# Kernel tuning notes

Measured on AMD Instinct MI355X. Metric: run time of the kernel, lower is better.

## Reference

```python
import jax, jax.numpy as jnp
import numpy as np


def setup_inputs() -> dict:
    key = jax.random.key(0)
    ks = jax.random.split(key, 8)
    B, C, H, W = 4, 256, 56, 56
    Cq = C // 8
    s = 0.05  # small init scale for conv weights, like kaiming-ish for 1x1 convs
    return {
        "x": jax.random.normal(ks[0], (B, C, H, W), jnp.float32),
        "Wq": jax.random.normal(ks[1], (Cq, C), jnp.float32) * s,
        "bq": jax.random.normal(ks[2], (Cq,), jnp.float32) * s,
        "Wk": jax.random.normal(ks[3], (Cq, C), jnp.float32) * s,
        "bk": jax.random.normal(ks[4], (Cq,), jnp.float32) * s,
        "Wv": jax.random.normal(ks[5], (C, C), jnp.float32) * s,
        "bv": jax.random.normal(ks[6], (C,), jnp.float32) * s,
        "gamma": jax.random.normal(ks[7], (1,), jnp.float32),
    }


def reference(x, Wq, bq, Wk, bk, Wv, bv, gamma):
    B, C, H, W = x.shape
    N = H * W
    xf = x.reshape(B, C, N)  # flatten spatial

    # 1x1 convs == channel matmuls
    q = jnp.einsum('oc,bcn->bon', Wq, xf) + bq[None, :, None]   # [B,Cq,N]
    k = jnp.einsum('oc,bcn->bon', Wk, xf) + bk[None, :, None]   # [B,Cq,N]
    v = jnp.einsum('oc,bcn->bon', Wv, xf) + bv[None, :, None]   # [B,C,N]

    # lipschitz_norm from weights: u=||Q||_F, v=max row-norm of K^T, w=max row-norm of V^T
    u = jnp.linalg.norm(Wq)
    vn = jnp.max(jnp.linalg.norm(Wk.T, axis=1))
    wn = jnp.max(jnp.linalg.norm(Wv.T, axis=1))
    norm_value = jnp.maximum(u * vn, u * wn)  # maximum(u*v, v*u, u*w)

    # energy[b,i,j] = <q[:,i], k[:,j]>, scaled by custom Lipschitz norm
    energy = jnp.einsum('bci,bcj->bij', q, k) / norm_value      # [B,N,N]
    attention = jax.nn.softmax(energy, axis=-1)

    # out[b,c,i] = sum_j v[b,c,j] * attention[b,i,j]
    out = jnp.einsum('bcj,bij->bci', v, attention).reshape(B, C, H, W)

    # lipschitz_bound: exp(sqrt(3)) * sqrt(N/C) + 2*sqrt(6)
    bound = np.float32(np.exp(np.sqrt(3.0)) * np.sqrt(N / C) + 2.0 * np.sqrt(6.0))
    out = out / bound

    return gamma * out + x
```

## Files before the change

### kernel.cpp

```cpp
#include <hip/hip_runtime.h>

#define N_SP 3136
#define C_CH 256
#define CQ   32
#define NB   4
#define JT   64
#define NJT  49
#define QT   64
#define INV_BOUND 0.04051569f
#define LOG2E 1.44269504f

typedef __attribute__((ext_vector_type(8))) short bf16x8;
typedef __attribute__((ext_vector_type(4))) float f32x4;
typedef __attribute__((ext_vector_type(2))) long long l64x2;
typedef unsigned short u16;
typedef unsigned int   u32;
typedef unsigned char  u8;
typedef long long      l64;

#define MFMA16(a,b,c) __builtin_amdgcn_mfma_f32_16x16x32_bf16(a,b,c,0,0,0)
#define MFMA8(a,b,c)  __builtin_amdgcn_mfma_f32_16x16x32_bf8_fp8(a,b,c,0,0,0)

__device__ __forceinline__ u16 f2b(float f) {
    u32 u = __builtin_bit_cast(u32, f);
    u += 0x7fffu + ((u >> 16) & 1u);
    return (u16)(u >> 16);
}
__device__ __forceinline__ u8 f2fp8(float f) {
    return (u8)(__builtin_amdgcn_cvt_pk_fp8_f32(f, f, 0, false) & 0xff);
}
__device__ __forceinline__ void dma16(const void* g, void* l) {
    __builtin_amdgcn_global_load_lds((const __attribute__((address_space(1))) u32*)g,
                                     (__attribute__((address_space(3))) u32*)l, 16, 0, 0);
}

__global__ __launch_bounds__(256) void stage0_kernel(
    const float* __restrict__ Wq, const float* __restrict__ Wk,
    const float* __restrict__ Wv, u8* __restrict__ Wqb,
    u8* __restrict__ Wkb, u8* __restrict__ Wvb,
    float* __restrict__ scale_out, float* __restrict__ kmax)
{
    __shared__ float red[256];
    const int t = threadIdx.x;
    const int bid = blockIdx.x;

    if (bid < 80) {
        int idx = bid * 256 + t;
        const float* src; u8* dst; int off;
        if (idx < 2048)      { src = Wq; dst = Wqb; off = idx; }
        else if (idx < 4096) { src = Wk; dst = Wkb; off = idx - 2048; }
        else                 { src = Wv; dst = Wvb; off = idx - 4096; }
        float4 v = *(const float4*)(src + off * 4);
        ushort4 o; o.x = f2b(v.x); o.y = f2b(v.y); o.z = f2b(v.z); o.w = f2b(v.w);
        const int row = off >> 6, inner = (off & 63) * 8;
        *(ushort4*)(dst + row * 512 + (inner ^ ((row & 15) << 5))) = o;
    } else {
        if (t < NB) kmax[t] = 0.f;
        float u2 = 0.f;
        for (int i = t; i < CQ * C_CH; i += 256) { float w = Wq[i]; u2 += w * w; }
        red[t] = u2; __syncthreads();
        #pragma unroll
        for (int s = 128; s > 0; s >>= 1) { if (t < s) red[t] += red[t + s]; __syncthreads(); }
        float u2t = red[0]; __syncthreads();
        float vn2 = 0.f;
        for (int o = 0; o < CQ; ++o)   { float w = Wk[o * C_CH + t]; vn2 += w * w; }
        float wn2 = 0.f;
        for (int o = 0; o < C_CH; ++o) { float w = Wv[o * C_CH + t]; wn2 += w * w; }
        red[t] = fmaxf(vn2, wn2); __syncthreads();
        #pragma unroll
        for (int s = 128; s > 0; s >>= 1) { if (t < s) red[t] = fmaxf(red[t], red[t + s]); __syncthreads(); }
        if (t == 0) scale_out[0] = 1.0f / (sqrtf(u2t) * sqrtf(red[0]));
    }
}

__global__ __launch_bounds__(512) void qkv_fused(
    const float* __restrict__ x, const u8* __restrict__ Wqb,
    const u8* __restrict__ Wkb, const u8* __restrict__ Wvb,
    const float* __restrict__ bq, const float* __restrict__ bk,
    const float* __restrict__ bv, const float* __restrict__ scale_p,
    u16* __restrict__ qT, u8* __restrict__ Kg, u8* __restrict__ Vg,
    float* __restrict__ qnorm, float* __restrict__ kmax)
{
    __shared__ __align__(16) u8 smem[147712];
    u8* const xTl = smem;
    float* const ftile = (float*)(smem + 32768);
    u8* const W0 = smem + 49408;
    u8* const W1 = smem + 82176;

    const int t = threadIdx.x;
    const int w = t >> 6, lane = t & 63, li = t & 15, g = (t >> 4) & 3;
    const int wq = w & 3, wh = w >> 2;
    const int b  = blockIdx.x / NJT;
    const int nt = blockIdx.x % NJT;
    const int n0 = nt * 64;
    const f32x4 zero = {0.f, 0.f, 0.f, 0.f};

    #pragma unroll
    for (int k = 0; k < 2; ++k)
        dma16(Wqb + k * 8192 + t * 16, W0 + k * 8192 + w * 1024);
    #pragma unroll
    for (int k = 0; k < 2; ++k)
        dma16(Wkb + k * 8192 + t * 16, W0 + 16384 + k * 8192 + w * 1024);
    #pragma unroll
    for (int k = 0; k < 8; ++k)
        dma16(Wvb + k * 8192 + t * 16, W1 + k * 8192 + w * 1024);

    #pragma unroll 1
    for (int sl = 0; sl < 4; ++sl) {
        const int c0 = sl * 64;
        if (t < 256) {
            const int cc = t >> 4, nn4 = (t & 15) * 4;
            #pragma unroll
            for (int k = 0; k < 4; ++k) {
                int cl = cc + k * 16;
                float4 v = *(const float4*)(x + (size_t)(b * C_CH + c0 + cl) * N_SP + n0 + nn4);
                ftile[cl * 65 + nn4]     = v.x;
                ftile[cl * 65 + nn4 + 1] = v.y;
                ftile[cl * 65 + nn4 + 2] = v.z;
                ftile[cl * 65 + nn4 + 3] = v.w;
            }
        }
        __syncthreads();
        if (t < 256) {
            const int c4 = (t & 15) * 4, nn = t >> 4;
            #pragma unroll
            for (int k = 0; k < 4; ++k) {
                int nl = nn + k * 16;
                ushort4 o;
                o.x = f2b(ftile[(c4 + 0) * 65 + nl]);
                o.y = f2b(ftile[(c4 + 1) * 65 + nl]);
                o.z = f2b(ftile[(c4 + 2) * 65 + nl]);
                o.w = f2b(ftile[(c4 + 3) * 65 + nl]);
                *(ushort4*)(xTl + nl * 512 + (((c0 + c4) * 2) ^ ((nl & 15) << 5))) = o;
            }
        }
        __syncthreads();
    }

    asm volatile("s_waitcnt vmcnt(0) lgkmcnt(0)" ::: "memory");
    __syncthreads();

    const int swz = li << 5;
    const int n = n0 + wq * 16 + li;
    bf16x8 xf[8];
    #pragma unroll
    for (int ks = 0; ks < 8; ++ks)
        xf[ks] = *(const bf16x8*)(xTl + (wq * 16 + li) * 512 + ((ks * 64 + 16 * g) ^ swz));

    if (wh == 0) {
        f32x4 aq0 = zero, aq1 = zero;
        #pragma unroll
        for (int ks = 0; ks < 8; ++ks) {
            const int o = (ks * 64 + 16 * g) ^ swz;
            bf16x8 w0 = *(const bf16x8*)(W0 + li * 512 + o);
            bf16x8 w1 = *(const bf16x8*)(W0 + (16 + li) * 512 + o);
            aq0 = MFMA16(w0, xf[ks], aq0);
            aq1 = MFMA16(w1, xf[ks], aq1);
        }
        const float scf = scale_p[0] * LOG2E;
        f32x4 bq0 = *(const f32x4*)(bq + 4 * g);
        f32x4 bq1 = *(const f32x4*)(bq + 16 + 4 * g);
        float qn2 = 0.f;
        ushort4 s0, s1;
        #pragma unroll
        for (int r = 0; r < 4; ++r) {
            float q0 = (aq0[r] + bq0[r]) * scf;
            float q1 = (aq1[r] + bq1[r]) * scf;
            qn2 += q0 * q0 + q1 * q1;
            ((u16*)&s0)[r] = f2b(q0); ((u16*)&s1)[r] = f2b(q1);
        }
        *(ushort4*)(qT + (size_t)(b * N_SP + n) * CQ + 4 * g)      = s0;
        *(ushort4*)(qT + (size_t)(b * N_SP + n) * CQ + 16 + 4 * g) = s1;
        qn2 += __shfl_xor(qn2, 16); qn2 += __shfl_xor(qn2, 32);
        if (g == 0) qnorm[b * N_SP + n] = sqrtf(qn2);
    } else {
        f32x4 ak0 = zero, ak1 = zero;
        #pragma unroll
        for (int ks = 0; ks < 8; ++ks) {
            const int o = (ks * 64 + 16 * g) ^ swz;
            bf16x8 w2 = *(const bf16x8*)(W0 + 16384 + li * 512 + o);
            bf16x8 w3 = *(const bf16x8*)(W0 + 16384 + (16 + li) * 512 + o);
            ak0 = MFMA16(w2, xf[ks], ak0);
            ak1 = MFMA16(w3, xf[ks], ak1);
        }
        f32x4 bk0 = *(const f32x4*)(bk + 4 * g);
        f32x4 bk1 = *(const f32x4*)(bk + 16 + 4 * g);
        float kn2 = 0.f;
        ushort4 s0, s1;
        #pragma unroll
        for (int r = 0; r < 4; ++r) {
            float k0 = ak0[r] + bk0[r];
            float k1 = ak1[r] + bk1[r];
            kn2 += k0 * k0 + k1 * k1;
            ((u16*)&s0)[r] = f2b(k0); ((u16*)&s1)[r] = f2b(k1);
        }
        u8* krow = Kg + ((size_t)b * N_SP + n) * 64;
        const int swn = ((n >> 1) & 3) << 4;
        *(ushort4*)(krow + ((8 * g) ^ swn))      = s0;
        *(ushort4*)(krow + ((32 + 8 * g) ^ swn)) = s1;
        kn2 += __shfl_xor(kn2, 16); kn2 += __shfl_xor(kn2, 32);
        float kn = sqrtf(kn2);
        #pragma unroll
        for (int d = 1; d < 16; d <<= 1) kn = fmaxf(kn, __shfl_xor(kn, d));
        if (lane == 0) atomicMax((int*)(kmax + b), __float_as_int(kn));
    }

    const int jj = wq * 16 + li;
    const int p = ((jj >> 5) & 1) * 8 + ((jj >> 3) & 3) * 16 + (jj & 7);
    u8* vtile = Vg + (size_t)(b * NJT + nt) * 16384;
    {
        const int r0 = wh * 64;
        f32x4 a[4] = {zero, zero, zero, zero};
        #pragma unroll
        for (int ks = 0; ks < 8; ++ks) {
            const int o = (ks * 64 + 16 * g) ^ swz;
            #pragma unroll
            for (int fr = 0; fr < 4; ++fr) {
                bf16x8 wf = *(const bf16x8*)(W1 + (size_t)(r0 + fr * 16 + li) * 512 + o);
                a[fr] = MFMA16(wf, xf[ks], a[fr]);
            }
        }
        #pragma unroll
        for (int fr = 0; fr < 4; ++fr) {
            f32x4 bb = *(const f32x4*)(bv + r0 + fr * 16 + 4 * g);
            #pragma unroll
            for (int r = 0; r < 4; ++r) {
                const int c = r0 + fr * 16 + 4 * g + r;
                vtile[c * 64 + (p ^ (((c >> 1) & 3) << 4))] = f2fp8(a[fr][r] + bb[r]);
            }
        }
    }

    __syncthreads();
    #pragma unroll
    for (int k = 0; k < 8; ++k)
        dma16(Wvb + 65536 + k * 8192 + t * 16, W1 + k * 8192 + w * 1024);
    asm volatile("s_waitcnt vmcnt(0)" ::: "memory");
    __syncthreads();

    {
        const int r0v = 128 + wh * 64;
        const int r0l = wh * 64;
        f32x4 a[4] = {zero, zero, zero, zero};
        #pragma unroll
        for (int ks = 0; ks < 8; ++ks) {
            const int o = (ks * 64 + 16 * g) ^ swz;
            #pragma unroll
            for (int fr = 0; fr < 4; ++fr) {
                bf16x8 wf = *(const bf16x8*)(W1 + (size_t)(r0l + fr * 16 + li) * 512 + o);
                a[fr] = MFMA16(wf, xf[ks], a[fr]);
            }
        }
        #pragma unroll
        for (int fr = 0; fr < 4; ++fr) {
            f32x4 bb = *(const f32x4*)(bv + r0v + fr * 16 + 4 * g);
            #pragma unroll
            for (int r = 0; r < 4; ++r) {
                const int c = r0v + fr * 16 + 4 * g + r;
                vtile[c * 64 + (p ^ (((c >> 1) & 3) << 4))] = f2fp8(a[fr][r] + bb[r]);
            }
        }
    }
}

__global__ __launch_bounds__(1024) void attn_mfma(
    const u16* __restrict__ qT, const u8* __restrict__ Kg,
    const u8* __restrict__ Vg, const float* __restrict__ x,
    const float* __restrict__ gamma_p, const float* __restrict__ qnorm,
    const float* __restrict__ kmax, float* __restrict__ out)
{
    __shared__ __align__(16) u8 smem[90112];
    u8* const Vl = smem;
    u8* const Kl = smem + 65536;
    u8* const Pl = smem + 81920;

    const int t = threadIdx.x;
    const int w = t >> 6, li = t & 15, g = (t >> 4) & 3;
    const int jh = w & 3, qh = w >> 2;
    const int swz = ((li >> 1) & 3) << 4;

    const int b  = blockIdx.x / NJT;
    const int qt = blockIdx.x % NJT;
    const int i0 = qt * QT;

    const u16* qTb = qT + (size_t)b * N_SP * CQ;
    const u8*  Kbb = Kg + (size_t)b * N_SP * 64;
    const u8*  Vbb = Vg + (size_t)b * NJT * 16384;
    const float kmb = kmax[b];
    const f32x4 zero = {0.f, 0.f, 0.f, 0.f};

    const bf16x8 qf = *(const bf16x8*)(qTb + (size_t)(i0 + qh * 16 + li) * CQ + 8 * g);
    const float  mr = qnorm[b * N_SP + i0 + qh * 16 + li] * kmb;

    f32x4 acc[4];
    #pragma unroll
    for (int qq = 0; qq < 4; ++qq) acc[qq] = zero;
    float ls = 0.f;

    #define ISSUE(jt_, s_) do {                                               \
        dma16(Vbb + (size_t)(jt_) * 16384 + t * 16,                           \
              Vl + (s_) * 16384 + w * 1024);                                  \
        if (t < 256)                                                          \
            dma16(Kbb + (size_t)(jt_) * 4096 + t * 16,                        \
                  Kl + (s_) * 4096 + w * 1024);                               \
    } while (0)

    #define SPHASE(it_) do {                                                  \
        const u8* Kc_ = Kl + ((it_) & 3) * 4096;                              \
        bf16x8 kf_ = *(const bf16x8*)(Kc_ + (jh * 16 + li) * 64 + ((16 * g) ^ swz)); \
        f32x4 s_ = MFMA16(kf_, qf, zero);                                     \
        float a0_ = exp2f(s_[0] - mr), a1_ = exp2f(s_[1] - mr);               \
        float a2_ = exp2f(s_[2] - mr), a3_ = exp2f(s_[3] - mr);               \
        ls += (a0_ + a1_) + (a2_ + a3_);                                      \
        int pk_ = __builtin_amdgcn_cvt_pk_bf8_f32(a0_, a1_, 0, false);        \
        pk_ = __builtin_amdgcn_cvt_pk_bf8_f32(a2_, a3_, pk_, true);           \
        *(u32*)(Pl + ((it_) & 1) * 4096 + (qh * 16 + li) * 64 + (p0 ^ swz)) = (u32)pk_; \
    } while (0)

    #define PVPHASE(it_) do {                                                 \
        const u8* Pp_ = Pl + ((it_) & 1) * 4096;                              \
        const u8* Vc_ = Vl + ((it_) & 3) * 16384;                             \
        __builtin_amdgcn_s_setprio(1);                                        \
        l64x2 pa0_ = *(const l64x2*)(Pp_ + (0 * 16 + li) * 64 + ((16 * g) ^ swz)); \
        l64x2 pa1_ = *(const l64x2*)(Pp_ + (1 * 16 + li) * 64 + ((16 * g) ^ swz)); \
        l64x2 pa2_ = *(const l64x2*)(Pp_ + (2 * 16 + li) * 64 + ((16 * g) ^ swz)); \
        l64x2 pa3_ = *(const l64x2*)(Pp_ + (3 * 16 + li) * 64 + ((16 * g) ^ swz)); \
        l64x2 v0_  = *(const l64x2*)(Vc_ + (w * 16 + li) * 64 + ((16 * g) ^ swz)); \
        acc[0] = MFMA8(pa0_[0], v0_[0], acc[0]);                              \
        acc[1] = MFMA8(pa1_[0], v0_[0], acc[1]);                              \
        acc[2] = MFMA8(pa2_[0], v0_[0], acc[2]);                              \
        acc[3] = MFMA8(pa3_[0], v0_[0], acc[3]);                              \
        acc[0] = MFMA8(pa0_[1], v0_[1], acc[0]);                              \
        acc[1] = MFMA8(pa1_[1], v0_[1], acc[1]);                              \
        acc[2] = MFMA8(pa2_[1], v0_[1], acc[2]);                              \
        acc[3] = MFMA8(pa3_[1], v0_[1], acc[3]);                              \
        __builtin_amdgcn_s_setprio(0);                                        \
    } while (0)

    ISSUE(0, 0);
    ISSUE(1, 1);

    const int p0 = ((jh >> 1) & 1) * 8 + ((jh * 2 + (g >> 1)) & 3) * 16 + 4 * (g & 1);

    if (w < 4) asm volatile("s_waitcnt vmcnt(2) lgkmcnt(0)" ::: "memory");
    else       asm volatile("s_waitcnt vmcnt(1) lgkmcnt(0)" ::: "memory");
    __builtin_amdgcn_s_barrier();
    asm volatile("" ::: "memory");
    ISSUE(2, 2);
    SPHASE(0);

    for (int it = 1; it < NJT; ++it) {
        if (w < 4) asm volatile("s_waitcnt vmcnt(2) lgkmcnt(0)" ::: "memory");
        else       asm volatile("s_waitcnt vmcnt(1) lgkmcnt(0)" ::: "memory");
        __builtin_amdgcn_s_barrier();
        asm volatile("" ::: "memory");
        {
            int jn = it + 2; if (jn > NJT - 1) jn = NJT - 1;
            ISSUE(jn, (it + 2) & 3);
        }
        PVPHASE(it - 1);
        SPHASE(it);
    }

    asm volatile("s_waitcnt lgkmcnt(0)" ::: "memory");
    __builtin_amdgcn_s_barrier();
    asm volatile("" ::: "memory");
    PVPHASE(NJT - 1);
    #undef ISSUE
    #undef SPHASE
    #undef PVPHASE

    ls += __shfl_xor(ls, 16); ls += __shfl_xor(ls, 32);
    __syncthreads();
    float* red       = (float*)Pl;
    float* red_final = (float*)(Pl + 1024);
    if ((t & 63) < 16) red[w * 16 + li] = ls;
    __syncthreads();
    if (t < 64) {
        const int qh2 = t >> 4, l2 = t & 15;
        float s = red[(qh2 * 4 + 0) * 16 + l2] + red[(qh2 * 4 + 1) * 16 + l2]
                + red[(qh2 * 4 + 2) * 16 + l2] + red[(qh2 * 4 + 3) * 16 + l2];
        red_final[t] = s;
    }
    __syncthreads();

    const float gsc = gamma_p[0] * INV_BOUND;
    const int c = w * 16 + li;
    #pragma unroll
    for (int qq = 0; qq < 4; ++qq) {
        f32x4 lsv = *(const f32x4*)(red_final + qq * 16 + 4 * g);
        f32x4 rinv;
        #pragma unroll
        for (int r = 0; r < 4; ++r) rinv[r] = gsc / lsv[r];
        const size_t base = ((size_t)b * C_CH + c) * N_SP + i0 + qq * 16 + 4 * g;
        float4 xv = *(const float4*)(x + base);
        float4 o;
        o.x = acc[qq][0] * rinv[0] + xv.x;
        o.y = acc[qq][1] * rinv[1] + xv.y;
        o.z = acc[qq][2] * rinv[2] + xv.z;
        o.w = acc[qq][3] * rinv[3] + xv.w;
        *(float4*)(out + base) = o;
    }
}

extern "C" void kernel_launch(void* const* d_in, const int* in_sizes, int n_in,
                              void* d_out, int out_size, void* d_ws, size_t ws_size,
                              hipStream_t stream)
{
    const float* x  = (const float*)d_in[0];
    const float* Wq = (const float*)d_in[1];
    const float* bq = (const float*)d_in[2];
    const float* Wk = (const float*)d_in[3];
    const float* bk = (const float*)d_in[4];
    const float* Wv = (const float*)d_in[5];
    const float* bv = (const float*)d_in[6];
    const float* gm = (const float*)d_in[7];
    float* out = (float*)d_out;
    float* ws  = (float*)d_ws;

    float* scale = ws;
    float* kmax  = ws + 4;
    float* qnorm = ws + 8;
    u8* Wqb = (u8*)(ws + 8 + NB * N_SP);
    u8* Wkb = Wqb + 32 * 512;
    u8* Wvb = Wkb + 32 * 512;
    u16* qT = (u16*)(Wvb + 256 * 512);
    u8* Kg  = (u8*)(qT + (size_t)NB * N_SP * CQ);
    u8* Vg  = Kg + (size_t)NB * N_SP * 64;

    stage0_kernel<<<81, 256, 0, stream>>>(Wq, Wk, Wv, Wqb, Wkb, Wvb, scale, kmax);
    qkv_fused<<<NB * NJT, 512, 0, stream>>>(x, Wqb, Wkb, Wvb, bq, bk, bv, scale, qT, Kg, Vg, qnorm, kmax);
    attn_mfma<<<NB * NJT, 1024, 0, stream>>>(qT, Kg, Vg, x, gm, qnorm, kmax, out);
}
```

Baseline: 81.32 us.

## Widen qkv_fused to 1024 threads with parallel x transpose and overlapped Wv load

The QKV projection kernel now runs 16 waves instead of 8. All four 64-channel slices of x are transposed into LDS at once rather than in a sequential four-pass loop. The first half of Wv is loaded by DMA into the freed staging buffer while Q/K are computed, and V rows are split across twice as many waves. This aims to cut the serial transpose latency and hide the weight load, at the cost of higher register pressure per thread under a 1024-thread launch bound and reuse of the staging buffer.

Measured after the change: 79.74 us (median of 2 runs). No clear change (-1.9%).

```diff
diff --git a/kernel.cpp b/kernel.cpp
--- a/kernel.cpp
+++ b/kernel.cpp
@@ -73,7 +73,7 @@
     }
 }
 
-__global__ __launch_bounds__(512) void qkv_fused(
+__global__ __launch_bounds__(1024) void qkv_fused(
     const float* __restrict__ x, const u8* __restrict__ Wqb,
     const u8* __restrict__ Wkb, const u8* __restrict__ Wvb,
     const float* __restrict__ bq, const float* __restrict__ bk,
@@ -81,15 +81,14 @@
     u16* __restrict__ qT, u8* __restrict__ Kg, u8* __restrict__ Vg,
     float* __restrict__ qnorm, float* __restrict__ kmax)
 {
-    __shared__ __align__(16) u8 smem[147712];
+    __shared__ __align__(16) u8 smem[132096];
     u8* const xTl = smem;
-    float* const ftile = (float*)(smem + 32768);
-    u8* const W0 = smem + 49408;
-    u8* const W1 = smem + 82176;
+    u8* const FW  = smem + 32768;
+    u8* const W0  = smem + 99328;
 
     const int t = threadIdx.x;
     const int w = t >> 6, lane = t & 63, li = t & 15, g = (t >> 4) & 3;
-    const int wq = w & 3, wh = w >> 2;
+    const int wq = w & 3;
     const int b  = blockIdx.x / NJT;
     const int nt = blockIdx.x % NJT;
     const int n0 = nt * 64;
@@ -97,48 +96,40 @@
 
     #pragma unroll
     for (int k = 0; k < 2; ++k)
-        dma16(Wqb + k * 8192 + t * 16, W0 + k * 8192 + w * 1024);
-    #pragma unroll
-    for (int k = 0; k < 2; ++k)
-        dma16(Wkb + k * 8192 + t * 16, W0 + 16384 + k * 8192 + w * 1024);
-    #pragma unroll
-    for (int k = 0; k < 8; ++k)
-        dma16(Wvb + k * 8192 + t * 16, W1 + k * 8192 + w * 1024);
-
-    #pragma unroll 1
-    for (int sl = 0; sl < 4; ++sl) {
+        dma16((k == 0 ? Wqb : Wkb) + t * 16, W0 + k * 16384 + w * 1024);
+
+    {
+        const int sl = t >> 8, tt = t & 255;
         const int c0 = sl * 64;
-        if (t < 256) {
-            const int cc = t >> 4, nn4 = (t & 15) * 4;
-            #pragma unroll
-            for (int k = 0; k < 4; ++k) {
-                int cl = cc + k * 16;
-                float4 v = *(const float4*)(x + (size_t)(b * C_CH + c0 + cl) * N_SP + n0 + nn4);
-                ftile[cl * 65 + nn4]     = v.x;
-                ftile[cl * 65 + nn4 + 1] = v.y;
-                ftile[cl * 65 + nn4 + 2] = v.z;
-                ftile[cl * 65 + nn4 + 3] = v.w;
-            }
+        float* ftile = (float*)(FW + sl * 16640);
+        const int cc = tt >> 4, nn4 = (tt & 15) * 4;
+        #pragma unroll
+        for (int k = 0; k < 4; ++k) {
+            int cl = cc + k * 16;
+            float4 v = *(const float4*)(x + (size_t)(b * C_CH + c0 + cl) * N_SP + n0 + nn4);
+            ftile[cl * 65 + nn4]     = v.x;
+            ftile[cl * 65 + nn4 + 1] = v.y;
+            ftile[cl * 65 + nn4 + 2] = v.z;
+            ftile[cl * 65 + nn4 + 3] = v.w;
         }
         __syncthreads();
-        if (t < 256) {
-            const int c4 = (t & 15) * 4, nn = t >> 4;
-            #pragma unroll
-            for (int k = 0; k < 4; ++k) {
-                int nl = nn + k * 16;
-                ushort4 o;
-                o.x = f2b(ftile[(c4 + 0) * 65 + nl]);
-                o.y = f2b(ftile[(c4 + 1) * 65 + nl]);
-                o.z = f2b(ftile[(c4 + 2) * 65 + nl]);
-                o.w = f2b(ftile[(c4 + 3) * 65 + nl]);
-                *(ushort4*)(xTl + nl * 512 + (((c0 + c4) * 2) ^ ((nl & 15) << 5))) = o;
-            }
-        }
-        __syncthreads();
-    }
-
-    asm volatile("s_waitcnt vmcnt(0) lgkmcnt(0)" ::: "memory");
-    __syncthreads();
+        const int c4 = (tt & 15) * 4, nn = tt >> 4;
+        #pragma unroll
+        for (int k = 0; k < 4; ++k) {
+            int nl = nn + k * 16;
+            ushort4 o;
+            o.x = f2b(ftile[(c4 + 0) * 65 + nl]);
+            o.y = f2b(ftile[(c4 + 1) * 65 + nl]);
+            o.z = f2b(ftile[(c4 + 2) * 65 + nl]);
+            o.w = f2b(ftile[(c4 + 3) * 65 + nl]);
+            *(ushort4*)(xTl + nl * 512 + (((c0 + c4) * 2) ^ ((nl & 15) << 5))) = o;
+        }
+    }
+    __syncthreads();
+
+    #pragma unroll
+    for (int k = 0; k < 4; ++k)
+        dma16(Wvb + k * 16384 + t * 16, FW + k * 16384 + w * 1024);
 
     const int swz = li << 5;
     const int n = n0 + wq * 16 + li;
@@ -147,81 +138,93 @@
     for (int ks = 0; ks < 8; ++ks)
         xf[ks] = *(const bf16x8*)(xTl + (wq * 16 + li) * 512 + ((ks * 64 + 16 * g) ^ swz));
 
-    if (wh == 0) {
-        f32x4 aq0 = zero, aq1 = zero;
-        #pragma unroll
-        for (int ks = 0; ks < 8; ++ks) {
-            const int o = (ks * 64 + 16 * g) ^ swz;
-            bf16x8 w0 = *(const bf16x8*)(W0 + li * 512 + o);
-            bf16x8 w1 = *(const bf16x8*)(W0 + (16 + li) * 512 + o);
-            aq0 = MFMA16(w0, xf[ks], aq0);
-            aq1 = MFMA16(w1, xf[ks], aq1);
-        }
-        const float scf = scale_p[0] * LOG2E;
-        f32x4 bq0 = *(const f32x4*)(bq + 4 * g);
-        f32x4 bq1 = *(const f32x4*)(bq + 16 + 4 * g);
-        float qn2 = 0.f;
-        ushort4 s0, s1;
-        #pragma unroll
-        for (int r = 0; r < 4; ++r) {
-            float q0 = (aq0[r] + bq0[r]) * scf;
-            float q1 = (aq1[r] + bq1[r]) * scf;
-            qn2 += q0 * q0 + q1 * q1;
-            ((u16*)&s0)[r] = f2b(q0); ((u16*)&s1)[r] = f2b(q1);
-        }
-        *(ushort4*)(qT + (size_t)(b * N_SP + n) * CQ + 4 * g)      = s0;
-        *(ushort4*)(qT + (size_t)(b * N_SP + n) * CQ + 16 + 4 * g) = s1;
-        qn2 += __shfl_xor(qn2, 16); qn2 += __shfl_xor(qn2, 32);
-        if (g == 0) qnorm[b * N_SP + n] = sqrtf(qn2);
-    } else {
-        f32x4 ak0 = zero, ak1 = zero;
-        #pragma unroll
-        for (int ks = 0; ks < 8; ++ks) {
-            const int o = (ks * 64 + 16 * g) ^ swz;
-            bf16x8 w2 = *(const bf16x8*)(W0 + 16384 + li * 512 + o);
-            bf16x8 w3 = *(const bf16x8*)(W0 + 16384 + (16 + li) * 512 + o);
-            ak0 = MFMA16(w2, xf[ks], ak0);
-            ak1 = MFMA16(w3, xf[ks], ak1);
-        }
-        f32x4 bk0 = *(const f32x4*)(bk + 4 * g);
-        f32x4 bk1 = *(const f32x4*)(bk + 16 + 4 * g);
-        float kn2 = 0.f;
-        ushort4 s0, s1;
-        #pragma unroll
-        for (int r = 0; r < 4; ++r) {
-            float k0 = ak0[r] + bk0[r];
-            float k1 = ak1[r] + bk1[r];
-            kn2 += k0 * k0 + k1 * k1;
-            ((u16*)&s0)[r] = f2b(k0); ((u16*)&s1)[r] = f2b(k1);
-        }
-        u8* krow = Kg + ((size_t)b * N_SP + n) * 64;
-        const int swn = ((n >> 1) & 3) << 4;
-        *(ushort4*)(krow + ((8 * g) ^ swn))      = s0;
-        *(ushort4*)(krow + ((32 + 8 * g) ^ swn)) = s1;
-        kn2 += __shfl_xor(kn2, 16); kn2 += __shfl_xor(kn2, 32);
-        float kn = sqrtf(kn2);
-        #pragma unroll
-        for (int d = 1; d < 16; d <<= 1) kn = fmaxf(kn, __shfl_xor(kn, d));
-        if (lane == 0) atomicMax((int*)(kmax + b), __float_as_int(kn));
-    }
+    asm volatile("s_waitcnt vmcnt(4) lgkmcnt(0)" ::: "memory");
+    __builtin_amdgcn_s_barrier();
+    asm volatile("" ::: "memory");
+
+    const int wh = w >> 2;
+    if (w < 8) {
+        if (wh == 0) {
+            f32x4 aq0 = zero, aq1 = zero;
+            #pragma unroll
+            for (int ks = 0; ks < 8; ++ks) {
+                const int o = (ks * 64 + 16 * g) ^ swz;
+                bf16x8 w0 = *(const bf16x8*)(W0 + li * 512 + o);
+                bf16x8 w1 = *(const bf16x8*)(W0 + (16 + li) * 512 + o);
+                aq0 = MFMA16(w0, xf[ks], aq0);
+                aq1 = MFMA16(w1, xf[ks], aq1);
+            }
+            const float scf = scale_p[0] * LOG2E;
+            f32x4 bq0 = *(const f32x4*)(bq + 4 * g);
+            f32x4 bq1 = *(const f32x4*)(bq + 16 + 4 * g);
+            float qn2 = 0.f;
+            ushort4 s0, s1;
+            #pragma unroll
+            for (int r = 0; r < 4; ++r) {
+                float q0 = (aq0[r] + bq0[r]) * scf;
+                float q1 = (aq1[r] + bq1[r]) * scf;
+                qn2 += q0 * q0 + q1 * q1;
+                ((u16*)&s0)[r] = f2b(q0); ((u16*)&s1)[r] = f2b(q1);
+            }
+            *(ushort4*)(qT + (size_t)(b * N_SP + n) * CQ + 4 * g)      = s0;
+            *(ushort4*)(qT + (size_t)(b * N_SP + n) * CQ + 16 + 4 * g) = s1;
+            qn2 += __shfl_xor(qn2, 16); qn2 += __shfl_xor(qn2, 32);
+            if (g == 0) qnorm[b * N_SP + n] = sqrtf(qn2);
+        } else {
+            f32x4 ak0 = zero, ak1 = zero;
+            #pragma unroll
+            for (int ks = 0; ks < 8; ++ks) {
+                const int o = (ks * 64 + 16 * g) ^ swz;
+                bf16x8 w2 = *(const bf16x8*)(W0 + 16384 + li * 512 + o);
+                bf16x8 w3 = *(const bf16x8*)(W0 + 16384 + (16 + li) * 512 + o);
+                ak0 = MFMA16(w2, xf[ks], ak0);
+                ak1 = MFMA16(w3, xf[ks], ak1);
+            }
+            f32x4 bk0 = *(const f32x4*)(bk + 4 * g);
+            f32x4 bk1 = *(const f32x4*)(bk + 16 + 4 * g);
+            float kn2 = 0.f;
+            ushort4 s0, s1;
+            #pragma unroll
+            for (int r = 0; r < 4; ++r) {
+                float k0 = ak0[r] + bk0[r];
+                float k1 = ak1[r] + bk1[r];
+                kn2 += k0 * k0 + k1 * k1;
+                ((u16*)&s0)[r] = f2b(k0); ((u16*)&s1)[r] = f2b(k1);
+            }
+            u8* krow = Kg + ((size_t)b * N_SP + n) * 64;
+            const int swn = ((n >> 1) & 3) << 4;
+            *(ushort4*)(krow + ((8 * g) ^ swn))      = s0;
+            *(ushort4*)(krow + ((32 + 8 * g) ^ swn)) = s1;
+            kn2 += __shfl_xor(kn2, 16); kn2 += __shfl_xor(kn2, 32);
+            float kn = sqrtf(kn2);
+            #pragma unroll
+            for (int d = 1; d < 16; d <<= 1) kn = fmaxf(kn, __shfl_xor(kn, d));
+            if (lane == 0) atomicMax((int*)(kmax + b), __float_as_int(kn));
+        }
+    }
+
+    asm volatile("s_waitcnt vmcnt(0)" ::: "memory");
+    __builtin_amdgcn_s_barrier();
+    asm volatile("" ::: "memory");
 
     const int jj = wq * 16 + li;
     const int p = ((jj >> 5) & 1) * 8 + ((jj >> 3) & 3) * 16 + (jj & 7);
     u8* vtile = Vg + (size_t)(b * NJT + nt) * 16384;
+    const int vg = w >> 2;
     {
-        const int r0 = wh * 64;
-        f32x4 a[4] = {zero, zero, zero, zero};
+        const int r0 = vg * 32;
+        f32x4 a[2] = {zero, zero};
         #pragma unroll
         for (int ks = 0; ks < 8; ++ks) {
             const int o = (ks * 64 + 16 * g) ^ swz;
             #pragma unroll
-            for (int fr = 0; fr < 4; ++fr) {
-                bf16x8 wf = *(const bf16x8*)(W1 + (size_t)(r0 + fr * 16 + li) * 512 + o);
+            for (int fr = 0; fr < 2; ++fr) {
+                bf16x8 wf = *(const bf16x8*)(FW + (size_t)(r0 + fr * 16 + li) * 512 + o);
                 a[fr] = MFMA16(wf, xf[ks], a[fr]);
             }
         }
         #pragma unroll
-        for (int fr = 0; fr < 4; ++fr) {
+        for (int fr = 0; fr < 2; ++fr) {
             f32x4 bb = *(const f32x4*)(bv + r0 + fr * 16 + 4 * g);
             #pragma unroll
             for (int r = 0; r < 4; ++r) {
@@ -233,26 +236,25 @@
 
     __syncthreads();
     #pragma unroll
-    for (int k = 0; k < 8; ++k)
-        dma16(Wvb + 65536 + k * 8192 + t * 16, W1 + k * 8192 + w * 1024);
+    for (int k = 0; k < 4; ++k)
+        dma16(Wvb + 65536 + k * 16384 + t * 16, FW + k * 16384 + w * 1024);
     asm volatile("s_waitcnt vmcnt(0)" ::: "memory");
     __syncthreads();
-
     {
-        const int r0v = 128 + wh * 64;
-        const int r0l = wh * 64;
-        f32x4 a[4] = {zero, zero, zero, zero};
+        const int r0v = 128 + vg * 32;
+        const int r0l = vg * 32;
+        f32x4 a[2] = {zero, zero};
         #pragma unroll
         for (int ks = 0; ks < 8; ++ks) {
             const int o = (ks * 64 + 16 * g) ^ swz;
             #pragma unroll
-            for (int fr = 0; fr < 4; ++fr) {
-                bf16x8 wf = *(const bf16x8*)(W1 + (size_t)(r0l + fr * 16 + li) * 512 + o);
+            for (int fr = 0; fr < 2; ++fr) {
+                bf16x8 wf = *(const bf16x8*)(FW + (size_t)(r0l + fr * 16 + li) * 512 + o);
                 a[fr] = MFMA16(wf, xf[ks], a[fr]);
             }
         }
         #pragma unroll
-        for (int fr = 0; fr < 4; ++fr) {
+        for (int fr = 0; fr < 2; ++fr) {
             f32x4 bb = *(const f32x4*)(bv + r0v + fr * 16 + 4 * g);
             #pragma unroll
             for (int r = 0; r < 4; ++r) {
@@ -429,6 +431,6 @@
     u8* Vg  = Kg + (size_t)NB * N_SP * 64;
 
     stage0_kernel<<<81, 256, 0, stream>>>(Wq, Wk, Wv, Wqb, Wkb, Wvb, scale, kmax);
-    qkv_fused<<<NB * NJT, 512, 0, stream>>>(x, Wqb, Wkb, Wvb, bq, bk, bv, scale, qT, Kg, Vg, qnorm, kmax);
+    qkv_fused<<<NB * NJT, 1024, 0, stream>>>(x, Wqb, Wkb, Wvb, bq, bk, bv, scale, qT, Kg, Vg, qnorm, kmax);
     attn_mfma<<<NB * NJT, 1024, 0, stream>>>(qT, Kg, Vg, x, gm, qnorm, kmax, out);
 }
```
